# Kernel tuning notes

Measured on AMD Instinct MI355X. Metric: run time of the kernel, lower is better.

## Reference

```python
import jax, jax.numpy as jnp
import numpy as np
from jax import lax

V, D, B, S = 50000, 300, 32, 128
H = 1024          # LSTM hidden per direction
NT = 9            # number of CRF tags
BN_EPS = 1e-5


def setup_inputs() -> dict:
    key = jax.random.key(0)
    ks = iter(jax.random.split(key, 48))
    def nrm(shape, scale=0.05):
        return jax.random.normal(next(ks), shape, dtype=jnp.float32) * scale
    inp = {}
    inp["x"] = jax.random.randint(next(ks), (B, S), 0, V)
    inp["y"] = jax.random.randint(next(ks), (B, S), 0, NT)
    inp["mask"] = jnp.ones((B, S), dtype=bool)
    inp["emb"] = nrm((V, D), 0.1)
    inp["lin1_w"] = nrm((512, D)); inp["lin1_b"] = jnp.zeros((512,), jnp.float32)
    in_sizes = [512, 2 * H, 2 * H, 2 * H]
    for l, isz in enumerate(in_sizes):
        inp[f"wih{l}"] = nrm((2, 4 * H, isz))   # [dir, 4H, in]
        inp[f"whh{l}"] = nrm((2, 4 * H, H))
        inp[f"bias{l}"] = jnp.zeros((2, 4 * H), jnp.float32)  # b_ih + b_hh combined
    inp["bn_gamma"] = jnp.ones((2 * H,), jnp.float32)
    inp["bn_beta"] = jnp.zeros((2 * H,), jnp.float32)
    inp["lin2_w"] = nrm((NT, 2 * H)); inp["lin2_b"] = jnp.zeros((NT,), jnp.float32)
    inp["crf_start"] = nrm((NT,), 0.1)
    inp["crf_end"] = nrm((NT,), 0.1)
    inp["crf_trans"] = nrm((NT, NT), 0.1)
    return inp


def _lstm_dir(xs, Wih, Whh, b):
    # xs: [S, B, in] -> hs: [S, B, H]; torch gate order i, f, g, o
    pre = jnp.einsum('sbi,gi->sbg', xs, Wih) + b  # [S,B,4H]
    h0 = jnp.zeros((xs.shape[1], Whh.shape[1]), xs.dtype)
    def step(carry, p):
        h, c = carry
        g = p + h @ Whh.T
        i, f, gg, o = jnp.split(g, 4, axis=-1)
        c = jax.nn.sigmoid(f) * c + jax.nn.sigmoid(i) * jnp.tanh(gg)
        h = jax.nn.sigmoid(o) * jnp.tanh(c)
        return (h, c), h
    _, hs = lax.scan(step, (h0, h0), pre)
    return hs


def _bilstm(xs, Wih, Whh, b):
    fwd = _lstm_dir(xs, Wih[0], Whh[0], b[0])
    bwd = _lstm_dir(xs[::-1], Wih[1], Whh[1], b[1])[::-1]
    return jnp.concatenate([fwd, bwd], axis=-1)


def _crf_llh(emis, tags, mask, start, end, trans):
    # torchcrf CRF forward, batch_first, reduction='sum'
    mf = mask.astype(emis.dtype)
    e_tag = jnp.take_along_axis(emis, tags[..., None], -1)[..., 0]  # [B,S]
    num = start[tags[:, 0]] + e_tag[:, 0]
    tr = trans[tags[:, :-1], tags[:, 1:]]                           # [B,S-1]
    num = num + jnp.sum(mf[:, 1:] * (tr + e_tag[:, 1:]), axis=1)
    lengths = mask.sum(axis=1).astype(jnp.int32)
    last_tag = jnp.take_along_axis(tags, (lengths - 1)[:, None], 1)[:, 0]
    num = num + end[last_tag]
    # forward algorithm (log-sum-exp recurrence over seq)
    alpha0 = start + emis[:, 0]                                     # [B,NT]
    seq_e = jnp.transpose(emis[:, 1:], (1, 0, 2))                   # [S-1,B,NT]
    seq_m = jnp.transpose(mask[:, 1:], (1, 0))                      # [S-1,B]
    def step(alpha, inp):
        e_t, m_t = inp
        nxt = jax.nn.logsumexp(alpha[:, :, None] + trans[None] + e_t[:, None, :], axis=1)
        return jnp.where(m_t[:, None], nxt, alpha), None
    alpha, _ = lax.scan(step, alpha0, (seq_e, seq_m))
    den = jax.nn.logsumexp(alpha + end, axis=1)
    return jnp.sum(num - den)


def reference(x, y, mask, emb, lin1_w, lin1_b,
              wih0, whh0, bias0, wih1, whh1, bias1,
              wih2, whh2, bias2, wih3, whh3, bias3,
              bn_gamma, bn_beta, lin2_w, lin2_b,
              crf_start, crf_end, crf_trans):
    h = emb[x]                          # [B,S,D]
    h = h @ lin1_w.T + lin1_b           # [B,S,512]
    hs = jnp.transpose(h, (1, 0, 2))    # [S,B,512]
    for Wih, Whh, bb in ((wih0, whh0, bias0), (wih1, whh1, bias1),
                         (wih2, whh2, bias2), (wih3, whh3, bias3)):
        hs = _bilstm(hs, Wih, Whh, bb)  # [S,B,2048]
    h = jnp.transpose(hs, (1, 0, 2))    # [B,S,2048]
    # BatchNorm1d eval (running mean 0, var 1) -> affine; ReLU; Dropout eval = id
    h = jax.nn.relu(bn_gamma * h / jnp.sqrt(jnp.float32(1.0 + BN_EPS)) + bn_beta)
    emis = h @ lin2_w.T + lin2_b        # [B,S,9]
    return _crf_llh(emis, y, mask, crf_start, crf_end, crf_trans)
```

## Files before the change

### kernel.cpp

```cpp
#include <hip/hip_runtime.h>
#include <hip/hip_bf16.h>

typedef __attribute__((ext_vector_type(8))) short short8;
typedef __attribute__((ext_vector_type(4))) float f32x4;
typedef unsigned short ushort_t;
typedef unsigned long long u64_t;

__device__ __forceinline__ ushort_t f2bf(float f) {
    __hip_bfloat16 h = __float2bfloat16(f);
    return *(ushort_t*)&h;
}
__device__ __forceinline__ float bf2f(ushort_t u) {
    union { float f; unsigned u32; } x; x.u32 = ((unsigned)u) << 16; return x.f;
}
__device__ __forceinline__ float sigmoidf_(float x) { return 1.0f / (1.0f + expf(-x)); }

__device__ __forceinline__ short8 cvt8(const float* p) {
    short8 r;
    #pragma unroll
    for (int j = 0; j < 8; j++) r[j] = (short)f2bf(p[j]);
    return r;
}

__global__ void lin1_pad(const float* __restrict__ w, ushort_t* __restrict__ d) {
    int idx = blockIdx.x * 256 + threadIdx.x;
    if (idx >= 512 * 320) return;
    int n = idx / 320, k = idx % 320;
    d[idx] = (k < 300) ? f2bf(w[n * 300 + k]) : (ushort_t)0;
}

__global__ void wcvt(const float* __restrict__ w, ushort_t* __restrict__ d, int n) {
    int idx = (blockIdx.x * 256 + threadIdx.x) * 8;
    if (idx >= n) return;
    float tmp[8];
    *(float4*)&tmp[0] = *(const float4*)(w + idx);
    *(float4*)&tmp[4] = *(const float4*)(w + idx + 4);
    *(short8*)&d[idx] = cvt8(tmp);
}

__global__ void emb_gather(const int* __restrict__ x, const float* __restrict__ emb,
                           ushort_t* __restrict__ XE) {
    int tok = blockIdx.x;
    int s = tok >> 5, b = tok & 31;
    int row = x[b * 128 + s];
    const float* e = emb + (size_t)row * 300;
    for (int d = threadIdx.x; d < 320; d += 64)
        XE[(size_t)tok * 320 + d] = (d < 300) ? f2bf(e[d]) : (ushort_t)0;
}

template<bool WF32, bool F32OUT, bool PERM>
__global__ __launch_bounds__(256) void gemm_bias(
    const ushort_t* __restrict__ X, const void* __restrict__ Wv,
    const float* __restrict__ bias, void* __restrict__ Cv,
    int K, int ldx, int ldw, int ldc)
{
    __shared__ __align__(16) ushort_t As[4 * 64 * 8];
    __shared__ __align__(16) ushort_t Bs[4 * 64 * 8];
    const int tid = threadIdx.x;
    const int lane = tid & 63;
    const int w = tid >> 6;
    const int wm = w & 1, wn = w >> 1;
    const int m0 = blockIdx.x * 64, n0 = blockIdx.y * 64;
    const int mt = tid >> 6;
    const int r = lane & 15, q = lane >> 4;
    const ushort_t* xsrc = X + (size_t)(m0 + mt * 16 + r) * ldx + q * 8;
    const ushort_t* wsrcb = WF32 ? nullptr : (const ushort_t*)Wv + (size_t)(n0 + mt * 16 + r) * ldw + q * 8;
    const float*    wsrcf = WF32 ? (const float*)Wv + (size_t)(n0 + mt * 16 + r) * ldw + q * 8 : nullptr;
    f32x4 acc00 = {0,0,0,0}, acc01 = {0,0,0,0}, acc10 = {0,0,0,0}, acc11 = {0,0,0,0};
    for (int k0 = 0; k0 < K; k0 += 32) {
        __syncthreads();
        *(uint4*)&As[(mt * 64 + lane) * 8] = *(const uint4*)(xsrc + k0);
        if (WF32) {
            float tmp[8];
            *(float4*)&tmp[0] = *(const float4*)(wsrcf + k0);
            *(float4*)&tmp[4] = *(const float4*)(wsrcf + k0 + 4);
            *(short8*)&Bs[(mt * 64 + lane) * 8] = cvt8(tmp);
        } else {
            *(uint4*)&Bs[(mt * 64 + lane) * 8] = *(const uint4*)(wsrcb + k0);
        }
        __syncthreads();
        short8 a0 = *(const short8*)&As[((2 * wm    ) * 64 + lane) * 8];
        short8 a1 = *(const short8*)&As[((2 * wm + 1) * 64 + lane) * 8];
        short8 b0 = *(const short8*)&Bs[((2 * wn    ) * 64 + lane) * 8];
        short8 b1 = *(const short8*)&Bs[((2 * wn + 1) * 64 + lane) * 8];
        acc00 = __builtin_amdgcn_mfma_f32_16x16x32_bf16(a0, b0, acc00, 0, 0, 0);
        acc01 = __builtin_amdgcn_mfma_f32_16x16x32_bf16(a0, b1, acc01, 0, 0, 0);
        acc10 = __builtin_amdgcn_mfma_f32_16x16x32_bf16(a1, b0, acc10, 0, 0, 0);
        acc11 = __builtin_amdgcn_mfma_f32_16x16x32_bf16(a1, b1, acc11, 0, 0, 0);
    }
    const int mb = m0 + wm * 32, nb = n0 + wn * 32;
    f32x4 accs[2][2] = {{acc00, acc01}, {acc10, acc11}};
    for (int i = 0; i < 2; i++)
        for (int j = 0; j < 2; j++) {
            int n = nb + j * 16 + r;
            float bv = bias[n];
            if (PERM) {
                int dirn = n >> 12, c = n & 4095;
                int gate = c >> 10, unit = c & 1023;
                int slice = unit >> 5, ue5 = unit & 31;
                int pos = ((ue5 & 15) << 1) | (ue5 >> 4);
                float* base = (float*)Cv + ((size_t)(dirn * 32 + slice) * 128) * 4096 + gate * 32 + pos;
                #pragma unroll
                for (int reg = 0; reg < 4; reg++) {
                    int m = mb + i * 16 + q * 4 + reg;
                    int ss = m >> 5, bb = m & 31;
                    base[(size_t)ss * 4096 + bb * 128] = accs[i][j][reg] + bv;
                }
            } else {
                #pragma unroll
                for (int reg = 0; reg < 4; reg++) {
                    int m = mb + i * 16 + q * 4 + reg;
                    float v = accs[i][j][reg] + bv;
                    if (F32OUT) ((float*)Cv)[(size_t)m * ldc + n] = v;
                    else ((ushort_t*)Cv)[(size_t)m * ldc + n] = f2bf(v);
                }
            }
        }
}

__device__ __forceinline__ void gbar(unsigned* flags, int dir, int slice, int epoch) {
    __syncthreads();
    if (threadIdx.x == 0)
        __hip_atomic_store(&flags[(dir * 32 + slice) * 16], (unsigned)epoch,
                           __ATOMIC_RELAXED, __HIP_MEMORY_SCOPE_AGENT);
    if (threadIdx.x < 64) {
        const unsigned* f = &flags[(dir * 32 + (threadIdx.x & 31)) * 16];
        int spins = 0;
        while (true) {
            unsigned v = __hip_atomic_load(f, __ATOMIC_RELAXED, __HIP_MEMORY_SCOPE_AGENT);
            if (__all(v >= (unsigned)epoch)) break;
            __builtin_amdgcn_s_sleep(1);
            if (++spins >= 65536) {
                spins = 0;
                v = __hip_atomic_load(f, __ATOMIC_ACQUIRE, __HIP_MEMORY_SCOPE_AGENT);
                if (__all(v >= (unsigned)epoch)) break;
            }
        }
    }
    __syncthreads();
}

__global__ __launch_bounds__(512) void lstm_scan(
    const float* __restrict__ PRE,
    const float* __restrict__ WHH,
    ushort_t* __restrict__ H,
    ushort_t* __restrict__ OUT,
    unsigned* __restrict__ flags,
    int epoch0)
{
    const int tid = threadIdx.x;
    const int lane = tid & 63;
    const int w = tid >> 6;
    const int dir = blockIdx.x >> 5;
    const int slice = blockIdx.x & 31;
    const int u0 = slice * 32;
    __shared__ __align__(16) ushort_t Af[2 * 32 * 64 * 8];
    __shared__ float gl[32 * 132];

    const int colw = w * 16 + (lane & 15);
    short8 bfr[32];
    {
        const int gate = colw >> 5, unit = colw & 31;
        const float* wrow = WHH + ((size_t)(dir * 4096 + gate * 1024 + u0 + unit)) * 1024 + (lane >> 4) * 8;
        #pragma unroll
        for (int kc = 0; kc < 32; kc++) {
            float tmp[8];
            *(float4*)&tmp[0] = *(const float4*)(wrow + kc * 32);
            *(float4*)&tmp[4] = *(const float4*)(wrow + kc * 32 + 4);
            bfr[kc] = cvt8(tmp);
        }
    }
    const int eb = tid >> 4, eu = tid & 15;
    float cst0 = 0.f, cst1 = 0.f;
    if ((eu & 1) == 0) {
        ushort_t* hz = H + (size_t)((0 * 2 + dir) * 32 + eb) * 1024 + u0;
        __hip_atomic_store((unsigned*)(hz + eu),      0u, __ATOMIC_RELAXED, __HIP_MEMORY_SCOPE_AGENT);
        __hip_atomic_store((unsigned*)(hz + 16 + eu), 0u, __ATOMIC_RELAXED, __HIP_MEMORY_SCOPE_AGENT);
    }
    const float* pbase = PRE + ((size_t)(dir * 32 + slice) * 128) * 4096 + eb * 128 + (eu << 1);
    float2 pb0, pb1, pb2, pb3;
    {
        const float* pp = pbase + (size_t)(dir ? 127 : 0) * 4096;
        pb0 = *(const float2*)(pp);
        pb1 = *(const float2*)(pp + 32);
        pb2 = *(const float2*)(pp + 64);
        pb3 = *(const float2*)(pp + 96);
    }
    int epoch = epoch0 + 1;
    gbar(flags, dir, slice, epoch);

    for (int t = 0; t < 128; t++) {
        const int s = dir ? (127 - t) : t;
        const int bufr = t & 1, bufw = bufr ^ 1;
        const ushort_t* Hsrc = H + (size_t)((bufr * 2 + dir) * 32) * 1024;
        u64_t tmp[16];
        #pragma unroll
        for (int i = 0; i < 8; i++) {
            int c = tid + i * 512;
            int ln = c & 63;
            int kc = (c >> 6) & 31;
            int mt2 = c >> 11;
            int b = mt2 * 16 + (ln & 15);
            int k = kc * 32 + (ln >> 4) * 8;
            const u64_t* src = (const u64_t*)(Hsrc + (size_t)b * 1024 + k);
            tmp[2 * i]     = __hip_atomic_load(src,     __ATOMIC_RELAXED, __HIP_MEMORY_SCOPE_AGENT);
            tmp[2 * i + 1] = __hip_atomic_load(src + 1, __ATOMIC_RELAXED, __HIP_MEMORY_SCOPE_AGENT);
        }
        #pragma unroll
        for (int i = 0; i < 8; i++) {
            int c = tid + i * 512;
            *(u64_t*)&Af[(size_t)c * 8]     = tmp[2 * i];
            *(u64_t*)&Af[(size_t)c * 8 + 4] = tmp[2 * i + 1];
        }
        __syncthreads();
        f32x4 acc0 = {0,0,0,0}, acc1 = {0,0,0,0};
        #pragma unroll
        for (int kc = 0; kc < 32; kc++) {
            short8 a0 = *(const short8*)&Af[(size_t)((     kc) * 64 + lane) * 8];
            short8 a1 = *(const short8*)&Af[(size_t)((32 + kc) * 64 + lane) * 8];
            acc0 = __builtin_amdgcn_mfma_f32_16x16x32_bf16(a0, bfr[kc], acc0, 0, 0, 0);
            acc1 = __builtin_amdgcn_mfma_f32_16x16x32_bf16(a1, bfr[kc], acc1, 0, 0, 0);
        }
        const int rowb = (lane >> 4) * 4;
        #pragma unroll
        for (int reg = 0; reg < 4; reg++) {
            gl[(rowb + reg) * 132 + colw]        = acc0[reg];
            gl[(16 + rowb + reg) * 132 + colw]   = acc1[reg];
        }
        __syncthreads();
        {
            float gi0 = gl[eb * 132 +   0 + eu] + pb0.x;
            float gi1 = gl[eb * 132 +  16 + eu] + pb0.y;
            float gf0 = gl[eb * 132 +  32 + eu] + pb1.x;
            float gf1 = gl[eb * 132 +  48 + eu] + pb1.y;
            float gg0 = gl[eb * 132 +  64 + eu] + pb2.x;
            float gg1 = gl[eb * 132 +  80 + eu] + pb2.y;
            float go0 = gl[eb * 132 +  96 + eu] + pb3.x;
            float go1 = gl[eb * 132 + 112 + eu] + pb3.y;
            if (t < 127) {
                const float* pp = pbase + (size_t)(dir ? (126 - t) : (t + 1)) * 4096;
                pb0 = *(const float2*)(pp);
                pb1 = *(const float2*)(pp + 32);
                pb2 = *(const float2*)(pp + 64);
                pb3 = *(const float2*)(pp + 96);
            }
            cst0 = sigmoidf_(gf0) * cst0 + sigmoidf_(gi0) * tanhf(gg0);
            cst1 = sigmoidf_(gf1) * cst1 + sigmoidf_(gi1) * tanhf(gg1);
            float h0 = sigmoidf_(go0) * tanhf(cst0);
            float h1 = sigmoidf_(go1) * tanhf(cst1);
            ushort_t hb0 = f2bf(h0), hb1 = f2bf(h1);
            unsigned o0 = (unsigned)(ushort_t)__shfl_xor((int)(unsigned)hb0, 1);
            unsigned o1 = (unsigned)(ushort_t)__shfl_xor((int)(unsigned)hb1, 1);
            if ((eu & 1) == 0) {
                ushort_t* hw = H + (size_t)((bufw * 2 + dir) * 32 + eb) * 1024 + u0;
                __hip_atomic_store((unsigned*)(hw + eu),      (unsigned)hb0 | (o0 << 16),
                                   __ATOMIC_RELAXED, __HIP_MEMORY_SCOPE_AGENT);
                __hip_atomic_store((unsigned*)(hw + 16 + eu), (unsigned)hb1 | (o1 << 16),
                                   __ATOMIC_RELAXED, __HIP_MEMORY_SCOPE_AGENT);
            }
            ushort_t* op = OUT + ((size_t)(s * 32 + eb)) * 2048 + (size_t)dir * 1024 + u0;
            op[eu] = hb0;
            op[16 + eu] = hb1;
        }
        epoch++;
        gbar(flags, dir, slice, epoch);
    }
}

__global__ __launch_bounds__(256) void emis_kernel(
    const ushort_t* __restrict__ Xf,
    const float* __restrict__ gamma, const float* __restrict__ beta,
    const float* __restrict__ w2, const float* __restrict__ b2,
    float* __restrict__ EM)
{
    const int lane = threadIdx.x & 63;
    const int wv = threadIdx.x >> 6;
    const int tok = blockIdx.x * 4 + wv;
    const int s = tok >> 5, b = tok & 31;
    const float inv = 0.9999950000374997f;
    const int j0 = lane * 4;
    float hn[32];
    #pragma unroll
    for (int c = 0; c < 8; c++) {
        int j = j0 + c * 256;
        u64_t xv = *(const u64_t*)(Xf + (size_t)tok * 2048 + j);
        float4 gv = *(const float4*)(gamma + j);
        float4 bv = *(const float4*)(beta + j);
        float x0 = bf2f((ushort_t)(xv      )), x1 = bf2f((ushort_t)(xv >> 16));
        float x2 = bf2f((ushort_t)(xv >> 32)), x3 = bf2f((ushort_t)(xv >> 48));
        float h0 = gv.x * x0 * inv + bv.x;
        float h1 = gv.y * x1 * inv + bv.y;
        float h2 = gv.z * x2 * inv + bv.z;
        float h3 = gv.w * x3 * inv + bv.w;
        hn[c * 4 + 0] = h0 > 0.f ? h0 : 0.f;
        hn[c * 4 + 1] = h1 > 0.f ? h1 : 0.f;
        hn[c * 4 + 2] = h2 > 0.f ? h2 : 0.f;
        hn[c * 4 + 3] = h3 > 0.f ? h3 : 0.f;
    }
    float acc[9];
    #pragma unroll
    for (int k = 0; k < 9; k++) {
        const float* wr = w2 + (size_t)k * 2048 + j0;
        float a = 0.f;
        #pragma unroll
        for (int c = 0; c < 8; c++) {
            float4 wv4 = *(const float4*)(wr + c * 256);
            a += hn[c * 4 + 0] * wv4.x + hn[c * 4 + 1] * wv4.y
               + hn[c * 4 + 2] * wv4.z + hn[c * 4 + 3] * wv4.w;
        }
        acc[k] = a;
    }
    #pragma unroll
    for (int k = 0; k < 9; k++) {
        #pragma unroll
        for (int off = 32; off > 0; off >>= 1)
            acc[k] += __shfl_xor(acc[k], off);
    }
    if (lane == 0) {
        float* em = EM + ((size_t)b * 128 + s) * 9;
        #pragma unroll
        for (int k = 0; k < 9; k++) em[k] = acc[k] + b2[k];
    }
}

__global__ __launch_bounds__(512) void crf_kernel(
    const float* __restrict__ EM,
    const int* __restrict__ y,
    const float* __restrict__ start, const float* __restrict__ endw,
    const float* __restrict__ trans,
    float* __restrict__ out)
{
    __shared__ float tr[81], st[9], en[9];
    __shared__ float alpha[2][32][12];
    __shared__ float numsh[32], densh[32];
    int tid = threadIdx.x;
    if (tid < 81) tr[tid] = trans[tid];
    if (tid < 9) { st[tid] = start[tid]; en[tid] = endw[tid]; }
    __syncthreads();
    if (tid < 32) {
        int b = tid;
        const int* yb = y + b * 128;
        const float* ebm = EM + (size_t)b * 1152;
        float num = st[yb[0]] + ebm[yb[0]];
        for (int s = 1; s < 128; s++)
            num += tr[yb[s - 1] * 9 + yb[s]] + ebm[s * 9 + yb[s]];
        num += en[yb[127]];
        numsh[b] = num;
    }
    int b = tid / 9, k = tid % 9;
    bool act = tid < 288;
    if (act) alpha[0][b][k] = st[k] + EM[(size_t)b * 1152 + k];
    __syncthreads();
    for (int s = 1; s < 128; s++) {
        int cur = s & 1, prv = cur ^ 1;
        if (act) {
            float m = -1e30f;
            #pragma unroll
            for (int j = 0; j < 9; j++)
                m = fmaxf(m, alpha[prv][b][j] + tr[j * 9 + k]);
            float sum = 0.f;
            #pragma unroll
            for (int j = 0; j < 9; j++)
                sum += expf(alpha[prv][b][j] + tr[j * 9 + k] - m);
            alpha[cur][b][k] = m + logf(sum) + EM[(size_t)b * 1152 + s * 9 + k];
        }
        __syncthreads();
    }
    if (tid < 32) {
        float m = -1e30f;
        for (int j = 0; j < 9; j++) m = fmaxf(m, alpha[1][tid][j] + en[j]);
        float sum = 0.f;
        for (int j = 0; j < 9; j++) sum += expf(alpha[1][tid][j] + en[j] - m);
        densh[tid] = m + logf(sum);
    }
    __syncthreads();
    if (tid == 0) {
        float tot = 0.f;
        for (int bb = 0; bb < 32; bb++) tot += numsh[bb] - densh[bb];
        out[0] = tot;
    }
}

extern "C" void kernel_launch(void* const* d_in, const int* in_sizes, int n_in,
                              void* d_out, int out_size, void* d_ws, size_t ws_size,
                              hipStream_t stream) {
    const int*   x       = (const int*)d_in[0];
    const int*   y       = (const int*)d_in[1];
    const float* emb     = (const float*)d_in[3];
    const float* lin1_w  = (const float*)d_in[4];
    const float* lin1_b  = (const float*)d_in[5];
    const float* wih[4]  = {(const float*)d_in[6],  (const float*)d_in[9],
                            (const float*)d_in[12], (const float*)d_in[15]};
    const float* whh[4]  = {(const float*)d_in[7],  (const float*)d_in[10],
                            (const float*)d_in[13], (const float*)d_in[16]};
    const float* biasl[4]= {(const float*)d_in[8],  (const float*)d_in[11],
                            (const float*)d_in[14], (const float*)d_in[17]};
    const float* bn_g    = (const float*)d_in[18];
    const float* bn_b    = (const float*)d_in[19];
    const float* lin2_w  = (const float*)d_in[20];
    const float* lin2_b  = (const float*)d_in[21];
    const float* crf_s   = (const float*)d_in[22];
    const float* crf_e   = (const float*)d_in[23];
    const float* crf_t   = (const float*)d_in[24];

    char* ws = (char*)d_ws;
    size_t off = 0;
    auto alloc = [&](size_t bytes) { size_t r = off; off += (bytes + 255) & ~(size_t)255; return r; };
    size_t oFLG  = alloc(4096);
    size_t oXE   = alloc((size_t)4096 * 320 * 2);
    size_t oWL1  = alloc((size_t)512 * 320 * 2);
    size_t oXB0  = alloc((size_t)4096 * 2048 * 2);
    size_t oXB1  = alloc((size_t)4096 * 2048 * 2);
    size_t oPRE  = alloc((size_t)4096 * 8192 * 4);
    size_t oH    = alloc((size_t)2 * 2 * 32 * 1024 * 2);
    size_t oEM   = alloc((size_t)32 * 128 * 9 * 4);
    size_t oWB   = alloc((size_t)8192 * 2048 * 2);
    (void)ws_size; (void)in_sizes; (void)n_in; (void)out_size;

    unsigned* flags = (unsigned*)(ws + oFLG);
    ushort_t* XE   = (ushort_t*)(ws + oXE);
    ushort_t* WL1  = (ushort_t*)(ws + oWL1);
    ushort_t* XB0  = (ushort_t*)(ws + oXB0);
    ushort_t* XB1  = (ushort_t*)(ws + oXB1);
    float*    PRE  = (float*)(ws + oPRE);
    ushort_t* Hb   = (ushort_t*)(ws + oH);
    float*    EM   = (float*)(ws + oEM);
    ushort_t* WB   = (ushort_t*)(ws + oWB);

    hipMemsetAsync(ws + oFLG, 0, 4096, stream);
    emb_gather<<<4096, 64, 0, stream>>>(x, emb, XE);
    lin1_pad<<<(512 * 320 + 255) / 256, 256, 0, stream>>>(lin1_w, WL1);
    gemm_bias<false, false, false><<<dim3(64, 8), 256, 0, stream>>>(XE, WL1, lin1_b, XB0, 320, 320, 320, 512);

    for (int l = 0; l < 4; l++) {
        int Kl = (l == 0) ? 512 : 2048;
        ushort_t* Xin  = (l % 2 == 0) ? XB0 : XB1;
        ushort_t* Xout = (l % 2 == 0) ? XB1 : XB0;
        int nw = 8192 * Kl;
        wcvt<<<nw / 2048, 256, 0, stream>>>(wih[l], WB, nw);
        gemm_bias<false, true, true><<<dim3(64, 128), 256, 0, stream>>>(Xin, WB, biasl[l], PRE,
                                                                        Kl, Kl, Kl, 8192);
        lstm_scan<<<64, 512, 0, stream>>>(PRE, whh[l], Hb, Xout, flags, l * 129);
    }
    emis_kernel<<<1024, 256, 0, stream>>>(XB0, bn_g, bn_b, lin2_w, lin2_b, EM);
    crf_kernel<<<1, 512, 0, stream>>>(EM, y, crf_s, crf_e, crf_t, (float*)d_out);
}
```

Before: 5.682 ms.

## Replace LSTM flag barrier with epoch-tagged hidden-state words and triple buffering

Drops the per-step global flag barrier in the recurrent scan. Each bf16 hidden value is now stored in a 32-bit word whose upper half carries an epoch tag, and readers poll the hidden buffer directly until every word has the expected tag. A third hidden buffer is added so writers cannot overwrite data that slow readers still need, and the LDS staging layout is padded. This aims to remove the barrier round-trip latency on every step, at the cost of twice the hidden-state traffic and a spin-polling loop over 32 loads per thread.

```diff
diff --git a/kernel.cpp b/kernel.cpp
--- a/kernel.cpp
+++ b/kernel.cpp
@@ -118,34 +118,11 @@
         }
 }
 
-__device__ __forceinline__ void gbar(unsigned* flags, int dir, int slice, int epoch) {
-    __syncthreads();
-    if (threadIdx.x == 0)
-        __hip_atomic_store(&flags[(dir * 32 + slice) * 16], (unsigned)epoch,
-                           __ATOMIC_RELAXED, __HIP_MEMORY_SCOPE_AGENT);
-    if (threadIdx.x < 64) {
-        const unsigned* f = &flags[(dir * 32 + (threadIdx.x & 31)) * 16];
-        int spins = 0;
-        while (true) {
-            unsigned v = __hip_atomic_load(f, __ATOMIC_RELAXED, __HIP_MEMORY_SCOPE_AGENT);
-            if (__all(v >= (unsigned)epoch)) break;
-            __builtin_amdgcn_s_sleep(1);
-            if (++spins >= 65536) {
-                spins = 0;
-                v = __hip_atomic_load(f, __ATOMIC_ACQUIRE, __HIP_MEMORY_SCOPE_AGENT);
-                if (__all(v >= (unsigned)epoch)) break;
-            }
-        }
-    }
-    __syncthreads();
-}
-
 __global__ __launch_bounds__(512) void lstm_scan(
     const float* __restrict__ PRE,
     const float* __restrict__ WHH,
-    ushort_t* __restrict__ H,
+    unsigned* __restrict__ H32,
     ushort_t* __restrict__ OUT,
-    unsigned* __restrict__ flags,
     int epoch0)
 {
     const int tid = threadIdx.x;
@@ -154,7 +131,7 @@
     const int dir = blockIdx.x >> 5;
     const int slice = blockIdx.x & 31;
     const int u0 = slice * 32;
-    __shared__ __align__(16) ushort_t Af[2 * 32 * 64 * 8];
+    __shared__ __align__(16) ushort_t Af[64 * 520];
     __shared__ float gl[32 * 132];
 
     const int colw = w * 16 + (lane & 15);
@@ -172,10 +149,11 @@
     }
     const int eb = tid >> 4, eu = tid & 15;
     float cst0 = 0.f, cst1 = 0.f;
-    if ((eu & 1) == 0) {
-        ushort_t* hz = H + (size_t)((0 * 2 + dir) * 32 + eb) * 1024 + u0;
-        __hip_atomic_store((unsigned*)(hz + eu),      0u, __ATOMIC_RELAXED, __HIP_MEMORY_SCOPE_AGENT);
-        __hip_atomic_store((unsigned*)(hz + 16 + eu), 0u, __ATOMIC_RELAXED, __HIP_MEMORY_SCOPE_AGENT);
+    {
+        unsigned tg0 = (unsigned)(epoch0 & 0xFFFF) << 16;
+        unsigned* hz = H32 + ((size_t)((0 * 2 + dir) * 32 + eb)) * 1024 + u0;
+        __hip_atomic_store(hz + eu,      tg0, __ATOMIC_RELAXED, __HIP_MEMORY_SCOPE_AGENT);
+        __hip_atomic_store(hz + eu + 16, tg0, __ATOMIC_RELAXED, __HIP_MEMORY_SCOPE_AGENT);
     }
     const float* pbase = PRE + ((size_t)(dir * 32 + slice) * 128) * 4096 + eb * 128 + (eu << 1);
     float2 pb0, pb1, pb2, pb3;
@@ -186,38 +164,49 @@
         pb2 = *(const float2*)(pp + 64);
         pb3 = *(const float2*)(pp + 96);
     }
-    int epoch = epoch0 + 1;
-    gbar(flags, dir, slice, epoch);
-
+    const int stg_base = (tid >> 4) * 520 + ((tid >> 2) & 3) * 128 + (tid & 3) * 2;
+    unsigned* Afu = (unsigned*)Af;
+
+    int br = 0;
     for (int t = 0; t < 128; t++) {
         const int s = dir ? (127 - t) : t;
-        const int bufr = t & 1, bufw = bufr ^ 1;
-        const ushort_t* Hsrc = H + (size_t)((bufr * 2 + dir) * 32) * 1024;
-        u64_t tmp[16];
-        #pragma unroll
-        for (int i = 0; i < 8; i++) {
-            int c = tid + i * 512;
-            int ln = c & 63;
-            int kc = (c >> 6) & 31;
-            int mt2 = c >> 11;
-            int b = mt2 * 16 + (ln & 15);
-            int k = kc * 32 + (ln >> 4) * 8;
-            const u64_t* src = (const u64_t*)(Hsrc + (size_t)b * 1024 + k);
-            tmp[2 * i]     = __hip_atomic_load(src,     __ATOMIC_RELAXED, __HIP_MEMORY_SCOPE_AGENT);
-            tmp[2 * i + 1] = __hip_atomic_load(src + 1, __ATOMIC_RELAXED, __HIP_MEMORY_SCOPE_AGENT);
-        }
-        #pragma unroll
-        for (int i = 0; i < 8; i++) {
-            int c = tid + i * 512;
-            *(u64_t*)&Af[(size_t)c * 8]     = tmp[2 * i];
-            *(u64_t*)&Af[(size_t)c * 8 + 4] = tmp[2 * i + 1];
+        const int bufr = br, bufw = (br == 2) ? 0 : br + 1;
+        const unsigned want = (unsigned)((epoch0 + t) & 0xFFFF);
+        const unsigned tagw = (unsigned)((epoch0 + t + 1) & 0xFFFF) << 16;
+        const u64_t* Hu = (const u64_t*)(H32 + ((size_t)(bufr * 2 + dir) * 32) * 1024);
+        unsigned pend = 0xFFFFFFFFu;
+        int spins = 0;
+        while (true) {
+            u64_t hv[32];
+            #pragma unroll
+            for (int g = 0; g < 32; g++)
+                if (pend & (1u << g))
+                    hv[g] = __hip_atomic_load(Hu + g * 512 + tid, __ATOMIC_RELAXED, __HIP_MEMORY_SCOPE_AGENT);
+            #pragma unroll
+            for (int g = 0; g < 32; g++)
+                if (pend & (1u << g)) {
+                    unsigned t0 = (unsigned)(hv[g] >> 16) & 0xFFFFu;
+                    unsigned t1 = (unsigned)(hv[g] >> 48);
+                    if (t0 == want && t1 == want) {
+                        unsigned pk = ((unsigned)hv[g] & 0xFFFFu) |
+                                      (((unsigned)(hv[g] >> 32) & 0xFFFFu) << 16);
+                        Afu[(stg_base + (g >> 4) * 16640 + (g & 15) * 8) >> 1] = pk;
+                        pend &= ~(1u << g);
+                    }
+                }
+            if (!pend) break;
+            __builtin_amdgcn_s_sleep(1);
+            if (++spins >= 16384) {
+                spins = 0;
+                (void)__hip_atomic_load(Hu + tid, __ATOMIC_ACQUIRE, __HIP_MEMORY_SCOPE_AGENT);
+            }
         }
         __syncthreads();
         f32x4 acc0 = {0,0,0,0}, acc1 = {0,0,0,0};
         #pragma unroll
         for (int kc = 0; kc < 32; kc++) {
-            short8 a0 = *(const short8*)&Af[(size_t)((     kc) * 64 + lane) * 8];
-            short8 a1 = *(const short8*)&Af[(size_t)((32 + kc) * 64 + lane) * 8];
+            short8 a0 = *(const short8*)&Af[kc * 520 + lane * 8];
+            short8 a1 = *(const short8*)&Af[(32 + kc) * 520 + lane * 8];
             acc0 = __builtin_amdgcn_mfma_f32_16x16x32_bf16(a0, bfr[kc], acc0, 0, 0, 0);
             acc1 = __builtin_amdgcn_mfma_f32_16x16x32_bf16(a1, bfr[kc], acc1, 0, 0, 0);
         }
@@ -249,21 +238,14 @@
             float h0 = sigmoidf_(go0) * tanhf(cst0);
             float h1 = sigmoidf_(go1) * tanhf(cst1);
             ushort_t hb0 = f2bf(h0), hb1 = f2bf(h1);
-            unsigned o0 = (unsigned)(ushort_t)__shfl_xor((int)(unsigned)hb0, 1);
-            unsigned o1 = (unsigned)(ushort_t)__shfl_xor((int)(unsigned)hb1, 1);
-            if ((eu & 1) == 0) {
-                ushort_t* hw = H + (size_t)((bufw * 2 + dir) * 32 + eb) * 1024 + u0;
-                __hip_atomic_store((unsigned*)(hw + eu),      (unsigned)hb0 | (o0 << 16),
-                                   __ATOMIC_RELAXED, __HIP_MEMORY_SCOPE_AGENT);
-                __hip_atomic_store((unsigned*)(hw + 16 + eu), (unsigned)hb1 | (o1 << 16),
-                                   __ATOMIC_RELAXED, __HIP_MEMORY_SCOPE_AGENT);
-            }
+            unsigned* hw = H32 + ((size_t)((bufw * 2 + dir) * 32 + eb)) * 1024 + u0;
+            __hip_atomic_store(hw + eu,      tagw | (unsigned)hb0, __ATOMIC_RELAXED, __HIP_MEMORY_SCOPE_AGENT);
+            __hip_atomic_store(hw + eu + 16, tagw | (unsigned)hb1, __ATOMIC_RELAXED, __HIP_MEMORY_SCOPE_AGENT);
             ushort_t* op = OUT + ((size_t)(s * 32 + eb)) * 2048 + (size_t)dir * 1024 + u0;
             op[eu] = hb0;
             op[16 + eu] = hb1;
         }
-        epoch++;
-        gbar(flags, dir, slice, epoch);
+        br = bufw;
     }
 }
 
@@ -406,28 +388,26 @@
     char* ws = (char*)d_ws;
     size_t off = 0;
     auto alloc = [&](size_t bytes) { size_t r = off; off += (bytes + 255) & ~(size_t)255; return r; };
-    size_t oFLG  = alloc(4096);
+    size_t oH32  = alloc((size_t)3 * 2 * 32 * 1024 * 4);
     size_t oXE   = alloc((size_t)4096 * 320 * 2);
     size_t oWL1  = alloc((size_t)512 * 320 * 2);
     size_t oXB0  = alloc((size_t)4096 * 2048 * 2);
     size_t oXB1  = alloc((size_t)4096 * 2048 * 2);
     size_t oPRE  = alloc((size_t)4096 * 8192 * 4);
-    size_t oH    = alloc((size_t)2 * 2 * 32 * 1024 * 2);
     size_t oEM   = alloc((size_t)32 * 128 * 9 * 4);
     size_t oWB   = alloc((size_t)8192 * 2048 * 2);
     (void)ws_size; (void)in_sizes; (void)n_in; (void)out_size;
 
-    unsigned* flags = (unsigned*)(ws + oFLG);
+    unsigned* H32  = (unsigned*)(ws + oH32);
     ushort_t* XE   = (ushort_t*)(ws + oXE);
     ushort_t* WL1  = (ushort_t*)(ws + oWL1);
     ushort_t* XB0  = (ushort_t*)(ws + oXB0);
     ushort_t* XB1  = (ushort_t*)(ws + oXB1);
     float*    PRE  = (float*)(ws + oPRE);
-    ushort_t* Hb   = (ushort_t*)(ws + oH);
     float*    EM   = (float*)(ws + oEM);
     ushort_t* WB   = (ushort_t*)(ws + oWB);
 
-    hipMemsetAsync(ws + oFLG, 0, 4096, stream);
+    hipMemsetAsync(ws + oH32, 0, (size_t)3 * 2 * 32 * 1024 * 4, stream);
     emb_gather<<<4096, 64, 0, stream>>>(x, emb, XE);
     lin1_pad<<<(512 * 320 + 255) / 256, 256, 0, stream>>>(lin1_w, WL1);
     gemm_bias<false, false, false><<<dim3(64, 8), 256, 0, stream>>>(XE, WL1, lin1_b, XB0, 320, 320, 320, 512);
@@ -440,7 +420,7 @@
         wcvt<<<nw / 2048, 256, 0, stream>>>(wih[l], WB, nw);
         gemm_bias<false, true, true><<<dim3(64, 128), 256, 0, stream>>>(Xin, WB, biasl[l], PRE,
                                                                         Kl, Kl, Kl, 8192);
-        lstm_scan<<<64, 512, 0, stream>>>(PRE, whh[l], Hb, Xout, flags, l * 129);
+        lstm_scan<<<64, 512, 0, stream>>>(PRE, whh[l], H32, Xout, 1 + l * 130);
     }
     emis_kernel<<<1024, 256, 0, stream>>>(XB0, bn_g, bn_b, lin2_w, lin2_b, EM);
     crf_kernel<<<1, 512, 0, stream>>>(EM, y, crf_s, crf_e, crf_t, (float*)d_out);
```

Result: slower. 6.250 ms (+10.0%).
